# Kernel tuning notes

Measured on AMD Instinct MI355X. Metric: run time of the kernel, lower is better.

Reference implementation:

```python
import jax, jax.numpy as jnp
import numpy as np

ROTARY_BASE = 10000
INFTY_APPROX = 1e30
B, T, M, H, D = 2, 2048, 2048, 16, 128


def rope(x):
    # x: [B, T, H, D]; half-split rotary encoding
    *_, length, _, width = x.shape
    half = width // 2
    positions = jnp.arange(length, dtype=jnp.float32)[None, :, None, None]      # [1,T,1,1]
    dims = jnp.arange(half, dtype=jnp.float32)
    ang_freqs = jnp.power(float(ROTARY_BASE), -dims / half)[None, None, None, :]  # [1,1,1,D/2]
    radians = positions * ang_freqs
    cos = jnp.cos(radians).astype(x.dtype)
    sin = jnp.sin(radians).astype(x.dtype)
    even, odd = x[..., :half], x[..., half:]
    r_even = even * cos - odd * sin
    r_odd = even * sin + odd * cos
    return jnp.concatenate([r_even, r_odd], axis=-1)


def setup_inputs() -> dict:
    key = jax.random.key(0)
    k0, k1, k2, k3, k4 = jax.random.split(key, 5)
    return {
        "x": jax.random.normal(k0, (B, T, M), dtype=jnp.float32),
        "w_aq": jax.random.normal(k1, (H, M, D), dtype=jnp.float32) * (M ** -0.5),
        "w_ak": jax.random.normal(k2, (H, M, D), dtype=jnp.float32) * (M ** -0.5),
        "w_av": jax.random.normal(k3, (H, M, D), dtype=jnp.float32) * (M ** -0.5),
        "w_ao": jax.random.normal(k4, (H, D, M), dtype=jnp.float32) * ((2 * 24 * M) ** -0.5),
    }


def reference(x, w_aq, w_ak, w_av, w_ao):
    q = jnp.einsum("btm,hmd->bthd", x, w_aq)
    k = jnp.einsum("btm,hmd->bthd", x, w_ak)
    v = jnp.einsum("btm,hmd->bthd", x, w_av)
    q = rope(q)
    k = rope(k)
    # muP attention scaling: 1/d_head (not 1/sqrt(d_head))
    mult = (1.0 / D) ** 0.5
    s = jnp.einsum("bihd,bjhd->bhij", mult * q, mult * k)  # [B,H,T,T]
    i = jnp.arange(T)[:, None]
    j = jnp.arange(T)[None, :]
    mask = (i < j)[None, None, :, :]  # mask future positions
    s = s - jnp.asarray(INFTY_APPROX, dtype=x.dtype) * mask
    p = jax.nn.softmax(s, axis=-1)
    o = jnp.einsum("bhij,bjhd->bihd", p, v)
    r = jnp.einsum("bihd,hdm->bim", o, w_ao)
    return r
```

## Files before the change

kernel.cpp:

```cpp
#include <hip/hip_runtime.h>

#define Bb 2
#define Tt 2048
#define Mm 2048
#define Hh 16
#define Dd 128

typedef __attribute__((ext_vector_type(8))) short bf16x8;
typedef __attribute__((ext_vector_type(4))) float f32x4;
typedef __attribute__((ext_vector_type(16))) float f32x16;

__device__ __forceinline__ unsigned short f2bf(float f) {
    unsigned int u = __builtin_bit_cast(unsigned int, f);
    u += 0x7FFFu + ((u >> 16) & 1u);
    return (unsigned short)(u >> 16);
}

__device__ __forceinline__ unsigned int cvt_pk_bf16(float lo, float hi) {
    unsigned int r;
    asm("v_cvt_pk_bf16_f32 %0, %1, %2" : "=v"(r) : "v"(lo), "v"(hi));
    return r;
}

__device__ __forceinline__ float fexp2(float x) { return __builtin_amdgcn_exp2f(x); }

__device__ __forceinline__ void gld16(const void* g, void* l) {
    __builtin_amdgcn_global_load_lds(
        (const __attribute__((address_space(1))) void*)g,
        (__attribute__((address_space(3))) void*)l, 16, 0, 0);
}


__global__ __launch_bounds__(256) void cvt_x2(const float* __restrict__ x,
                                              unsigned short* __restrict__ xb2) {
    const int blk = blockIdx.x;
    const int mt = blk >> 5, kt = blk & 31;
#pragma unroll
    for (int it = 0; it < 4; ++it) {
        int s = it * 256 + threadIdx.x;
        int row = ((s >> 6) & 3) * 32 + (s & 31);
        int k = (s >> 8) * 16 + ((s >> 5) & 1) * 8;
        const float* sp = x + ((long)(mt * 128 + row)) * 2048 + kt * 64 + k;
        float4 a = *(const float4*)sp;
        float4 b = *(const float4*)(sp + 4);
        uint4 pk;
        pk.x = (unsigned int)f2bf(a.x) | ((unsigned int)f2bf(a.y) << 16);
        pk.y = (unsigned int)f2bf(a.z) | ((unsigned int)f2bf(a.w) << 16);
        pk.z = (unsigned int)f2bf(b.x) | ((unsigned int)f2bf(b.y) << 16);
        pk.w = (unsigned int)f2bf(b.z) | ((unsigned int)f2bf(b.w) << 16);
        *(uint4*)(xb2 + (((long)(mt * 32 + kt)) * 1024 + s) * 8) = pk;
    }
}

__global__ __launch_bounds__(256) void w_qkv_tile(
    const float* __restrict__ wq, const float* __restrict__ wk, const float* __restrict__ wv,
    unsigned short* __restrict__ outBase) {
    __shared__ float tile[64][132];
    const int kt = blockIdx.x;
    const int zy = blockIdx.y;
    const int which = zy >> 4, head = zy & 15;
    const float* src = (which == 0 ? wq : which == 1 ? wk : wv) + (long)head * 2048 * 128;
    const int tid = threadIdx.x;
#pragma unroll
    for (int it = 0; it < 8; ++it) {
        int f = it * 256 + tid;
        int row = f >> 5, c4 = f & 31;
        float4 v = *(const float4*)(src + (long)(kt * 64 + row) * 128 + c4 * 4);
        tile[row][c4 * 4 + 0] = v.x;
        tile[row][c4 * 4 + 1] = v.y;
        tile[row][c4 * 4 + 2] = v.z;
        tile[row][c4 * 4 + 3] = v.w;
    }
    __syncthreads();
    unsigned short* outp = outBase + (((long)(which * 16 + head)) * 32 + kt) * 1024 * 8;
#pragma unroll
    for (int it = 0; it < 4; ++it) {
        int up = it * 256 + tid;
        int kk = up >> 8, nf = (up >> 6) & 3, l = up & 63;
        int il = l & 31, hl = l >> 5;
        int d = il + 64 * (nf & 1) + 32 * (nf >> 1);
        int kl = kk * 16 + hl * 8;
        uint4 pk;
        pk.x = (unsigned int)f2bf(tile[kl + 0][d]) | ((unsigned int)f2bf(tile[kl + 1][d]) << 16);
        pk.y = (unsigned int)f2bf(tile[kl + 2][d]) | ((unsigned int)f2bf(tile[kl + 3][d]) << 16);
        pk.z = (unsigned int)f2bf(tile[kl + 4][d]) | ((unsigned int)f2bf(tile[kl + 5][d]) << 16);
        pk.w = (unsigned int)f2bf(tile[kl + 6][d]) | ((unsigned int)f2bf(tile[kl + 7][d]) << 16);
        *(uint4*)(outp + (long)up * 8) = pk;
    }
}

__global__ __launch_bounds__(256) void transpose_cvt(const float* __restrict__ in,
                                                     unsigned short* __restrict__ out,
                                                     int rows, int cols,
                                                     long in_slab, long out_slab) {
    __shared__ float tile[32][33];
    const float* ip = in + (long)blockIdx.z * in_slab;
    unsigned short* op = out + (long)blockIdx.z * out_slab;
    int r0 = blockIdx.x * 32, c0 = blockIdx.y * 32;
    int tx = threadIdx.x & 31, ty = threadIdx.x >> 5;
#pragma unroll
    for (int j = 0; j < 32; j += 8)
        tile[ty + j][tx] = ip[(long)(r0 + ty + j) * cols + c0 + tx];
    __syncthreads();
#pragma unroll
    for (int j = 0; j < 32; j += 8)
        op[(long)(c0 + ty + j) * rows + r0 + tx] = f2bf(tile[tx][ty + j]);
}

__global__ __launch_bounds__(256) void rope_tab(float* __restrict__ cosT,
                                                float* __restrict__ sinT) {
    int idx = blockIdx.x * 256 + threadIdx.x;
    int t = idx >> 6, d = idx & 63;
    float freq = powf(10000.f, -(float)d / 64.f);
    float ang = (float)t * freq;
    sinT[idx] = sinf(ang);
    cosT[idx] = cosf(ang);
}

template <bool WIDE>
__device__ __forceinline__ void proj_sub9(
    const unsigned short* __restrict__ xb2,
    const unsigned short* __restrict__ wT2,
    char* lds, int bm, int offc,
    unsigned short* __restrict__ qO, unsigned short* __restrict__ kO,
    unsigned short* __restrict__ vtO,
    const float* __restrict__ cosT, const float* __restrict__ sinT, int tid) {
    const int lane = tid & 63, wave = tid >> 6;
    const int il = lane & 31, hl = lane >> 5;
    const int wm = WIDE ? (wave >> 2) : (wave >> 1);
    const int wn = WIDE ? (wave & 3) : (wave & 1);
    const int hseg0 = offc >> 7;
    const int mode = offc >> 11;
    constexpr int MF = WIDE ? 4 : 2;
    constexpr int NFR = WIDE ? 12 : 8;
    constexpr int FS = WIDE ? 6 : 4;

    f32x16 acc[MF][2];
#pragma unroll
    for (int a = 0; a < MF; ++a)
#pragma unroll
        for (int b2 = 0; b2 < 2; ++b2)
#pragma unroll
            for (int e = 0; e < 16; ++e) acc[a][b2][e] = 0.f;

    auto stageTo = [&](int bufOff, int kt2) {
        const int kt = kt2 >> 1, hf = kt2 & 1;
        char* dst = lds + bufOff;
#pragma unroll
        for (int i = 0; i < 2; ++i) {
            int f = i * 512 + tid;
            int kk = f >> 9, rf = (f >> 6) & 7, l = f & 63;
            int mt = 2 * bm + (rf >> 2), rb = rf & 3;
            gld16(xb2 + (((long)(mt * 32 + kt)) * 1024 + (2 * hf + kk) * 256 + rb * 64 + l) * 8,
                  dst + f * 16);
        }
        if (WIDE) {
#pragma unroll
            for (int i = 0; i < 2; ++i) {
                int g = i * 512 + tid;
                int kk = g >> 9, cf = (g >> 6) & 7, l = g & 63;
                int hs = hseg0 + (cf >> 2), nf = cf & 3;
                gld16(wT2 + (((long)(hs * 32 + kt)) * 1024 + (2 * hf + kk) * 256 + nf * 64 + l) * 8,
                      dst + 16384 + g * 16);
            }
        } else {
            int g = tid;
            int kk = g >> 8, nf = (g >> 6) & 3, l = g & 63;
            gld16(wT2 + (((long)(hseg0 * 32 + kt)) * 1024 + (2 * hf + kk) * 256 + nf * 64 + l) * 8,
                  dst + 16384 + g * 16);
        }
    };

    auto prefetch = [&](bf16x8 (&fr)[NFR], int bufOff) {
        const char* bc = lds + bufOff;
#pragma unroll
        for (int kk2 = 0; kk2 < 2; ++kk2) {
#pragma unroll
            for (int mf = 0; mf < MF; ++mf)
                fr[kk2 * FS + mf] = *(const bf16x8*)(bc + (kk2 * 512 + (wm * MF + mf) * 64 + lane) * 16);
#pragma unroll
            for (int nf = 0; nf < 2; ++nf)
                fr[kk2 * FS + MF + nf] = *(const bf16x8*)(bc + 16384 +
                    ((WIDE ? kk2 * 512 : kk2 * 256) + (wn * 2 + nf) * 64 + lane) * 16);
        }
    };

    auto domfma = [&](bf16x8 (&fr)[NFR]) {
        __builtin_amdgcn_s_setprio(1);
#pragma unroll
        for (int kk2 = 0; kk2 < 2; ++kk2)
#pragma unroll
            for (int mf = 0; mf < MF; ++mf)
#pragma unroll
                for (int nf = 0; nf < 2; ++nf)
                    acc[mf][nf] = __builtin_amdgcn_mfma_f32_32x32x16_bf16(
                        fr[kk2 * FS + mf], fr[kk2 * FS + MF + nf], acc[mf][nf], 0, 0, 0);
        __builtin_amdgcn_s_setprio(0);
    };

    bf16x8 fA[NFR], fB[NFR];

    stageTo(0, 0);
    stageTo(32768, 1);
    if (WIDE) asm volatile("s_waitcnt vmcnt(4)" ::: "memory");
    else      asm volatile("s_waitcnt vmcnt(3)" ::: "memory");
    __builtin_amdgcn_s_barrier();
    prefetch(fA, 0);

    int curOff = 0;
    for (int p = 0; p < 31; ++p) {
        {
            int preOff = curOff + 65536; if (preOff >= 98304) preOff -= 98304;
            stageTo(preOff, 2 * p + 2);
            if (WIDE) asm volatile("s_waitcnt vmcnt(4) lgkmcnt(0)" ::: "memory");
            else      asm volatile("s_waitcnt vmcnt(3) lgkmcnt(0)" ::: "memory");
            __builtin_amdgcn_s_barrier();
            int nxtOff = curOff + 32768; if (nxtOff >= 98304) nxtOff -= 98304;
            prefetch(fB, nxtOff);
            domfma(fA);
            curOff = nxtOff;
        }
        {
            int preOff = curOff + 65536; if (preOff >= 98304) preOff -= 98304;
            stageTo(preOff, 2 * p + 3);
            if (WIDE) asm volatile("s_waitcnt vmcnt(4) lgkmcnt(0)" ::: "memory");
            else      asm volatile("s_waitcnt vmcnt(3) lgkmcnt(0)" ::: "memory");
            __builtin_amdgcn_s_barrier();
            int nxtOff = curOff + 32768; if (nxtOff >= 98304) nxtOff -= 98304;
            prefetch(fA, nxtOff);
            domfma(fB);
            curOff = nxtOff;
        }
    }
    asm volatile("s_waitcnt vmcnt(0) lgkmcnt(0)" ::: "memory");
    __builtin_amdgcn_s_barrier();
    {
        int nxtOff = curOff + 32768; if (nxtOff >= 98304) nxtOff -= 98304;
        prefetch(fB, nxtOff);
        domfma(fA);
    }
    domfma(fB);

    const int b = bm >> 3;
    const int t0 = (bm & 7) * 256;
    const int head_g = WIDE ? (hseg0 + (wn >> 1)) : hseg0;
    const int head_l = head_g & 15;
    const int opar = WIDE ? (wn & 1) : wn;
    constexpr int WMS = WIDE ? 128 : 64;

    if (mode < 2) {
        const float qs = (mode == 0) ? 0.011271055f : 1.0f;
        unsigned short* outp = (mode == 0) ? qO : kO;
        long hb = ((long)(b * Hh + head_l)) * Tt;
        int d_lo = il + 32 * opar;
#pragma unroll
        for (int mf = 0; mf < MF; ++mf)
#pragma unroll
            for (int reg = 0; reg < 16; ++reg) {
                int r = (reg & 3) + 8 * (reg >> 2) + 4 * hl;
                int tt = t0 + wm * WMS + mf * 32 + r;
                float c = cosT[tt * 64 + d_lo], s = sinT[tt * 64 + d_lo];
                float ev = acc[mf][0][reg], od = acc[mf][1][reg];
                long base = (hb + tt) * Dd;
                outp[base + d_lo]      = f2bf((ev * c - od * s) * qs);
                outp[base + d_lo + 64] = f2bf((ev * s + od * c) * qs);
            }
    } else {
        __syncthreads();
        char* patch = lds + wave * 4096;
        long hdbase = ((long)(b * Hh + head_l)) * Dd * Tt;
#pragma unroll
        for (int mf = 0; mf < MF; ++mf) {
#pragma unroll
            for (int nf = 0; nf < 2; ++nf) {
                int dslot = nf * 32 + il;
                int swz = (dslot & 3) << 4;
#pragma unroll
                for (int qg = 0; qg < 4; ++qg) {
                    uint2 w;
                    w.x = cvt_pk_bf16(acc[mf][nf][qg * 4 + 0], acc[mf][nf][qg * 4 + 1]);
                    w.y = cvt_pk_bf16(acc[mf][nf][qg * 4 + 2], acc[mf][nf][qg * 4 + 3]);
                    *(uint2*)(patch + dslot * 64 + ((qg * 16 + hl * 8) ^ swz)) = w;
                }
            }
            __builtin_amdgcn_s_waitcnt(0);
#pragma unroll
            for (int p2 = 0; p2 < 4; ++p2) {
                int dslot = p2 * 16 + (lane >> 2);
                int t8 = lane & 3;
                uint4 v = *(const uint4*)(patch + dslot * 64 + ((t8 * 16) ^ ((dslot & 3) << 4)));
                int o = opar * 2 + (dslot >> 5), il2 = dslot & 31;
                int dd = il2 + 32 * (o >> 1) + 64 * (o & 1);
                int tg = t0 + wm * WMS + mf * 32 + t8 * 8;
                *(uint4*)(vtO + hdbase + (long)dd * Tt + tg) = v;
            }
            __builtin_amdgcn_s_waitcnt(0);
        }
    }
}

__global__ __launch_bounds__(512, 2) void proj_gemm9(
    const unsigned short* __restrict__ xb2,
    const unsigned short* __restrict__ wT2,
    unsigned short* __restrict__ qO,
    unsigned short* __restrict__ kO,
    unsigned short* __restrict__ vtO,
    const float* __restrict__ cosT,
    const float* __restrict__ sinT) {
    __shared__ __align__(16) char lds[98304];
    const int bm = blockIdx.x;
    const int bc = blockIdx.y;
    const int s = bc * 384;
    const bool swap = ((s & 2047) == 1920);
    const int offw = swap ? s + 128 : s;
    const int offn = swap ? s : s + 256;
    const int tid = threadIdx.x;

    proj_sub9<true>(xb2, wT2, lds, bm, offw, qO, kO, vtO, cosT, sinT, tid);
    __syncthreads();
    proj_sub9<false>(xb2, wT2, lds, bm, offn, qO, kO, vtO, cosT, sinT, tid);
}

__global__ __launch_bounds__(256) void attn_kernel(
    const unsigned short* __restrict__ q,
    const unsigned short* __restrict__ k,
    const unsigned short* __restrict__ vt,
    unsigned short* __restrict__ o) {
    __shared__ __align__(16) unsigned short lds[32768];

    const int lid = (int)blockIdx.x;
    const int p = lid & 255;
    const int bh = p & 31;
    const int q0 = p >> 5;
    const int qb = (lid >> 8) ? (15 - q0) : q0;

    const int tid = threadIdx.x, lane = tid & 63, wave = tid >> 6;
    const int h = lane >> 5, iln = lane & 31;

    const unsigned short* qp = q + (long)bh * Tt * Dd;
    const unsigned short* kp = k + (long)bh * Tt * Dd;
    const unsigned short* vp = vt + (long)bh * Dd * Tt;

    const int i_g = qb * 128 + wave * 32 + iln;
    bf16x8 qf[8];
#pragma unroll
    for (int kk = 0; kk < 8; ++kk)
        qf[kk] = *(const bf16x8*)(qp + (long)i_g * Dd + kk * 16 + h * 8);

    f32x16 accO[4];
#pragma unroll
    for (int nb = 0; nb < 4; ++nb)
#pragma unroll
        for (int e = 0; e < 16; ++e) accO[nb][e] = 0.f;

    float m_r = -1e30f, l_r = 0.f;
    const int ntiles = 2 * qb + 2;

    auto stage = [&](int buf, int tix) {
        const int j0s = tix * 64;
#pragma unroll
        for (int it = 0; it < 4; ++it) {
            int f = it * 256 + tid;
            int rk = f >> 4, ck = f & 15;
            gld16(kp + ((long)(j0s + rk) * Dd + ((ck ^ (rk & 7)) << 3)),
                  (char*)lds + buf * 16384 + f * 16);
            int rv = f >> 3, cv = f & 7;
            gld16(vp + ((long)rv * Tt + j0s + ((cv ^ (rv & 7)) << 3)),
                  (char*)lds + 32768 + buf * 16384 + f * 16);
        }
    };

    stage(0, 0);

    for (int tix = 0; tix < ntiles; ++tix) {
        const int cur = tix & 1;
        const int j0 = tix * 64;
        if (tix + 1 < ntiles) {
            stage(cur ^ 1, tix + 1);
            asm volatile("s_waitcnt vmcnt(8)" ::: "memory");
        } else {
            asm volatile("s_waitcnt vmcnt(0)" ::: "memory");
        }
        __builtin_amdgcn_s_barrier();

        const char* Kb = (const char*)lds + cur * 16384;
        const char* Vb = (const char*)lds + 32768 + cur * 16384;

        f32x16 sacc[2];
#pragma unroll
        for (int mb = 0; mb < 2; ++mb)
#pragma unroll
            for (int e = 0; e < 16; ++e) sacc[mb][e] = 0.f;

        __builtin_amdgcn_s_setprio(1);
#pragma unroll
        for (int mb = 0; mb < 2; ++mb) {
            int row = mb * 32 + iln;
            const char* Kr = Kb + row * 256;
            int sw = row & 7;
#pragma unroll
            for (int kk = 0; kk < 8; ++kk) {
                bf16x8 kf = *(const bf16x8*)(Kr + 16 * ((kk * 2 + h) ^ sw));
                sacc[mb] = __builtin_amdgcn_mfma_f32_32x32x16_bf16(kf, qf[kk], sacc[mb], 0, 0, 0);
            }
        }
        __builtin_amdgcn_s_setprio(0);

        const bool domask = (j0 + 63 > qb * 128);
        if (domask) {
#pragma unroll
            for (int mb = 0; mb < 2; ++mb)
#pragma unroll
                for (int reg = 0; reg < 16; ++reg) {
                    int j = j0 + mb * 32 + (reg & 3) + 8 * (reg >> 2) + 4 * h;
                    if (j > i_g) sacc[mb][reg] = -1e30f;
                }
        }

        float red[16];
#pragma unroll
        for (int r = 0; r < 16; ++r) red[r] = fmaxf(sacc[0][r], sacc[1][r]);
#pragma unroll
        for (int s = 8; s >= 1; s >>= 1)
#pragma unroll
            for (int r = 0; r < s; ++r) red[r] = fmaxf(red[r], red[r + s]);
        float mx = fmaxf(red[0], __shfl_xor(red[0], 32, 64));

        if (__any(mx > m_r + 8.f)) {
            float mn = fmaxf(m_r, mx);
            float corr = fexp2(m_r - mn);
            m_r = mn;
            l_r *= corr;
#pragma unroll
            for (int reg = 0; reg < 16; ++reg) {
                int rrow = (reg & 3) + 8 * (reg >> 2) + 4 * h;
                float c = __shfl(corr, rrow, 64);
#pragma unroll
                for (int nb = 0; nb < 4; ++nb) accO[nb][reg] *= c;
            }
        }

        float pe[2][16];
#pragma unroll
        for (int mb = 0; mb < 2; ++mb)
#pragma unroll
            for (int r = 0; r < 16; ++r) pe[mb][r] = fexp2(sacc[mb][r] - m_r);
        float sr[16];
#pragma unroll
        for (int r = 0; r < 16; ++r) sr[r] = pe[0][r] + pe[1][r];
#pragma unroll
        for (int s = 8; s >= 1; s >>= 1)
#pragma unroll
            for (int r = 0; r < s; ++r) sr[r] += sr[r + s];
        l_r += sr[0] + __shfl_xor(sr[0], 32, 64);

        unsigned int pu[2][8];
#pragma unroll
        for (int mb = 0; mb < 2; ++mb)
#pragma unroll
            for (int t = 0; t < 8; ++t)
                pu[mb][t] = cvt_pk_bf16(pe[mb][2 * t], pe[mb][2 * t + 1]);

        unsigned int rv2[2][4];
#pragma unroll
        for (int mb = 0; mb < 2; ++mb)
#pragma unroll
            for (int u = 0; u < 4; ++u) {
                unsigned int sv = h ? pu[mb][(u & 1) + 4 * (u >> 1)]
                                    : pu[mb][2 + (u & 1) + 4 * (u >> 1)];
                rv2[mb][u] = __shfl_xor(sv, 32, 64);
            }

        __builtin_amdgcn_s_setprio(1);
#pragma unroll
        for (int kk2 = 0; kk2 < 4; ++kk2) {
            const int mb = kk2 >> 1, c2 = kk2 & 1;
            unsigned int w0 = h ? rv2[mb][2 * c2 + 0] : pu[mb][4 * c2 + 0];
            unsigned int w1 = h ? rv2[mb][2 * c2 + 1] : pu[mb][4 * c2 + 1];
            unsigned int w2 = h ? pu[mb][4 * c2 + 2] : rv2[mb][2 * c2 + 0];
            unsigned int w3 = h ? pu[mb][4 * c2 + 3] : rv2[mb][2 * c2 + 1];
            uint4 aw; aw.x = w0; aw.y = w1; aw.z = w2; aw.w = w3;
            bf16x8 af = __builtin_bit_cast(bf16x8, aw);
#pragma unroll
            for (int nb = 0; nb < 4; ++nb) {
                int dd = nb * 32 + iln;
                int byte = dd * 128 + 16 * ((kk2 * 2 + h) ^ (dd & 7));
                bf16x8 vf = *(const bf16x8*)(Vb + byte);
                accO[nb] = __builtin_amdgcn_mfma_f32_32x32x16_bf16(af, vf, accO[nb], 0, 0, 0);
            }
        }
        __builtin_amdgcn_s_setprio(0);

        asm volatile("" ::: "memory");
        __builtin_amdgcn_s_barrier();
    }

    const int b = bh >> 4, hh = bh & 15;
    float invl = 1.f / l_r;
#pragma unroll
    for (int reg = 0; reg < 16; ++reg) {
        int rrow = (reg & 3) + 8 * (reg >> 2) + 4 * h;
        float iv = __shfl(invl, rrow, 64);
        int t = qb * 128 + wave * 32 + rrow;
        long base = ((long)(b * Tt + t) * Hh + hh) * Dd;
#pragma unroll
        for (int nb = 0; nb < 4; ++nb)
            o[base + nb * 32 + iln] = f2bf(accO[nb][reg] * iv);
    }
}

__global__ __launch_bounds__(256) void out_gemm(
    const unsigned short* __restrict__ oIn,
    const unsigned short* __restrict__ woT,
    float* __restrict__ out) {
    __shared__ __align__(16) unsigned short smem[32768];
    const int bm = blockIdx.x, bn = blockIdx.y;
    const int tid = threadIdx.x;
    const int lane = tid & 63;
    const int wave = tid >> 6;
    const int g = lane >> 4;
    const int ln = lane & 15;

    const unsigned short* arow = oIn + (long)bm * 128 * Mm;
    const unsigned short* brow = woT + (long)bn * 128 * Mm;

    f32x4 acc[2][8];
#pragma unroll
    for (int a = 0; a < 2; ++a)
#pragma unroll
        for (int b2 = 0; b2 < 8; ++b2)
#pragma unroll
            for (int e = 0; e < 4; ++e) acc[a][b2][e] = 0.f;

    auto stage = [&](int buf, int kt) {
        const int k0 = kt * 64;
#pragma unroll
        for (int it = 0; it < 4; ++it) {
            int f = it * 256 + tid;
            int r = f >> 3, c = f & 7;
            long off = (long)r * Mm + k0 + ((c ^ (r & 7)) << 3);
            gld16(arow + off, (char*)smem + buf * 32768 + f * 16);
            gld16(brow + off, (char*)smem + buf * 32768 + 16384 + f * 16);
        }
    };

    stage(0, 0);

    for (int kt = 0; kt < Mm / 64; ++kt) {
        const int cur = kt & 1;
        asm volatile("s_waitcnt vmcnt(0)" ::: "memory");
        __builtin_amdgcn_s_barrier();
        if (kt + 1 < Mm / 64) stage(cur ^ 1, kt + 1);

        const char* Ab = (const char*)smem + cur * 32768;
        const char* Bv = Ab + 16384;
#pragma unroll
        for (int kc = 0; kc < 2; ++kc) {
            bf16x8 af[2];
#pragma unroll
            for (int rf = 0; rf < 2; ++rf) {
                int row = wave * 32 + rf * 16 + ln;
                int byte = (row * 128 + kc * 64 + g * 16) ^ ((row & 7) << 4);
                af[rf] = *(const bf16x8*)(Ab + byte);
            }
#pragma unroll
            for (int ni = 0; ni < 8; ++ni) {
                int row = ni * 16 + ln;
                int byte = (row * 128 + kc * 64 + g * 16) ^ ((row & 7) << 4);
                bf16x8 bfv = *(const bf16x8*)(Bv + byte);
#pragma unroll
                for (int rf = 0; rf < 2; ++rf)
                    acc[rf][ni] = __builtin_amdgcn_mfma_f32_16x16x32_bf16(af[rf], bfv, acc[rf][ni], 0, 0, 0);
            }
        }
        asm volatile("" ::: "memory");
    }

#pragma unroll
    for (int rf = 0; rf < 2; ++rf)
#pragma unroll
        for (int reg = 0; reg < 4; ++reg) {
            long row = bm * 128 + wave * 32 + rf * 16 + g * 4 + reg;
#pragma unroll
            for (int ni = 0; ni < 8; ++ni)
                out[row * Mm + bn * 128 + ni * 16 + ln] = acc[rf][ni][reg];
        }
}


extern "C" void kernel_launch(void* const* d_in, const int* in_sizes, int n_in,
                              void* d_out, int out_size, void* d_ws, size_t ws_size,
                              hipStream_t stream) {
    const float* x    = (const float*)d_in[0];
    const float* w_aq = (const float*)d_in[1];
    const float* w_ak = (const float*)d_in[2];
    const float* w_av = (const float*)d_in[3];
    const float* w_ao = (const float*)d_in[4];
    float* out = (float*)d_out;

    char* ws = (char*)d_ws;
    const long SZ_BTM = 16777216;
    const long SZ_W   = 8388608;
    unsigned short* xb2 = (unsigned short*)(ws);
    unsigned short* qB  = (unsigned short*)(ws + SZ_BTM);
    unsigned short* kB  = (unsigned short*)(ws + 2 * SZ_BTM);
    unsigned short* vtB = (unsigned short*)(ws + 3 * SZ_BTM);
    unsigned short* oB  = (unsigned short*)(ws + 4 * SZ_BTM);
    unsigned short* wT2 = (unsigned short*)(ws + 5 * SZ_BTM);
    unsigned short* woT = (unsigned short*)(ws + 5 * SZ_BTM + 3 * SZ_W);
    float* cosT = (float*)(ws + 5 * SZ_BTM + 4 * SZ_W);
    float* sinT = (float*)(ws + 5 * SZ_BTM + 4 * SZ_W + 524288);

    cvt_x2<<<1024, 256, 0, stream>>>(x, xb2);
    w_qkv_tile<<<dim3(32, 48), 256, 0, stream>>>(w_aq, w_ak, w_av, wT2);
    transpose_cvt<<<dim3(64, 64, 1), 256, 0, stream>>>(w_ao, woT, 2048, 2048, 0, 0);
    rope_tab<<<512, 256, 0, stream>>>(cosT, sinT);

    proj_gemm9<<<dim3(16, 16), 512, 0, stream>>>(xb2, wT2, qB, kB, vtB, cosT, sinT);
    attn_kernel<<<dim3(512), 256, 0, stream>>>(qB, kB, vtB, oB);
    out_gemm<<<dim3(32, 16), 256, 0, stream>>>(oB, woT, out);
}
```

Baseline: 251.4 us.

## Restructure projection GEMM to double-buffered full-K-tile staging with direct LDS fragment loads

Replaces the triple-buffered half-tile pipeline, which used register prefetch of MFMA fragments, with a two-stage double buffer that loads a full K-tile (64 k) per iteration into 128KB of LDS. Fragments are read from LDS right before each MFMA group instead of being ping-ponged in registers. The goal is to halve the number of barriers per K iteration and cut register pressure. In exchange it uses more LDS per block, which may limit occupancy to one block per CU despite launch_bounds(512,2). It also exposes LDS read latency, since fragment loads are no longer overlapped with the previous MFMAs.

```diff
diff --git a/kernel.cpp b/kernel.cpp
--- a/kernel.cpp
+++ b/kernel.cpp
@@ -118,7 +118,7 @@
 }
 
 template <bool WIDE>
-__device__ __forceinline__ void proj_sub9(
+__device__ __forceinline__ void proj_sub10(
     const unsigned short* __restrict__ xb2,
     const unsigned short* __restrict__ wT2,
     char* lds, int bm, int offc,
@@ -132,8 +132,6 @@
     const int hseg0 = offc >> 7;
     const int mode = offc >> 11;
     constexpr int MF = WIDE ? 4 : 2;
-    constexpr int NFR = WIDE ? 12 : 8;
-    constexpr int FS = WIDE ? 6 : 4;
 
     f32x16 acc[MF][2];
 #pragma unroll
@@ -143,103 +141,73 @@
 #pragma unroll
             for (int e = 0; e < 16; ++e) acc[a][b2][e] = 0.f;
 
-    auto stageTo = [&](int bufOff, int kt2) {
-        const int kt = kt2 >> 1, hf = kt2 & 1;
-        char* dst = lds + bufOff;
-#pragma unroll
-        for (int i = 0; i < 2; ++i) {
+    auto stageTo = [&](int buf, int kt) {
+        char* dst = lds + buf * 65536;
+#pragma unroll
+        for (int i = 0; i < 4; ++i) {
             int f = i * 512 + tid;
-            int kk = f >> 9, rf = (f >> 6) & 7, l = f & 63;
-            int mt = 2 * bm + (rf >> 2), rb = rf & 3;
-            gld16(xb2 + (((long)(mt * 32 + kt)) * 1024 + (2 * hf + kk) * 256 + rb * 64 + l) * 8,
-                  dst + f * 16);
+            int sub = f >> 10, s = f & 1023;
+            gld16(xb2 + (((long)((2 * bm + sub) * 32 + kt)) * 1024 + s) * 8, dst + f * 16);
         }
         if (WIDE) {
+#pragma unroll
+            for (int i = 0; i < 4; ++i) {
+                int g = i * 512 + tid;
+                int hs = g >> 10, u = g & 1023;
+                gld16(wT2 + (((long)((hseg0 + hs) * 32 + kt)) * 1024 + u) * 8,
+                      dst + 32768 + g * 16);
+            }
+        } else {
 #pragma unroll
             for (int i = 0; i < 2; ++i) {
                 int g = i * 512 + tid;
-                int kk = g >> 9, cf = (g >> 6) & 7, l = g & 63;
-                int hs = hseg0 + (cf >> 2), nf = cf & 3;
-                gld16(wT2 + (((long)(hs * 32 + kt)) * 1024 + (2 * hf + kk) * 256 + nf * 64 + l) * 8,
-                      dst + 16384 + g * 16);
-            }
+                gld16(wT2 + (((long)(hseg0 * 32 + kt)) * 1024 + g) * 8,
+                      dst + 32768 + g * 16);
+            }
+        }
+    };
+
+    stageTo(0, 0);
+
+    for (int t = 0; t < 32; ++t) {
+        const int cur = t & 1;
+        if (t + 1 < 32) {
+            stageTo(cur ^ 1, t + 1);
+            if (WIDE) asm volatile("s_waitcnt vmcnt(8)" ::: "memory");
+            else      asm volatile("s_waitcnt vmcnt(6)" ::: "memory");
         } else {
-            int g = tid;
-            int kk = g >> 8, nf = (g >> 6) & 3, l = g & 63;
-            gld16(wT2 + (((long)(hseg0 * 32 + kt)) * 1024 + (2 * hf + kk) * 256 + nf * 64 + l) * 8,
-                  dst + 16384 + g * 16);
-        }
-    };
-
-    auto prefetch = [&](bf16x8 (&fr)[NFR], int bufOff) {
-        const char* bc = lds + bufOff;
-#pragma unroll
-        for (int kk2 = 0; kk2 < 2; ++kk2) {
+            asm volatile("s_waitcnt vmcnt(0)" ::: "memory");
+        }
+        __builtin_amdgcn_s_barrier();
+
+        const char* bc = lds + cur * 65536;
+        __builtin_amdgcn_s_setprio(1);
+#pragma unroll
+        for (int kk = 0; kk < 4; ++kk) {
+            bf16x8 af[MF], bf[2];
+#pragma unroll
+            for (int mf = 0; mf < MF; ++mf) {
+                int chunk = WIDE ? (wm * 1024 + kk * 256 + mf * 64 + lane)
+                                 : ((wm >> 1) * 1024 + kk * 256 + ((wm & 1) * 2 + mf) * 64 + lane);
+                af[mf] = *(const bf16x8*)(bc + chunk * 16);
+            }
+#pragma unroll
+            for (int nf2 = 0; nf2 < 2; ++nf2) {
+                int chunk = WIDE ? ((wn >> 1) * 1024 + kk * 256 + ((wn & 1) * 2 + nf2) * 64 + lane)
+                                 : (kk * 256 + (wn * 2 + nf2) * 64 + lane);
+                bf[nf2] = *(const bf16x8*)(bc + 32768 + chunk * 16);
+            }
 #pragma unroll
             for (int mf = 0; mf < MF; ++mf)
-                fr[kk2 * FS + mf] = *(const bf16x8*)(bc + (kk2 * 512 + (wm * MF + mf) * 64 + lane) * 16);
-#pragma unroll
-            for (int nf = 0; nf < 2; ++nf)
-                fr[kk2 * FS + MF + nf] = *(const bf16x8*)(bc + 16384 +
-                    ((WIDE ? kk2 * 512 : kk2 * 256) + (wn * 2 + nf) * 64 + lane) * 16);
-        }
-    };
-
-    auto domfma = [&](bf16x8 (&fr)[NFR]) {
-        __builtin_amdgcn_s_setprio(1);
-#pragma unroll
-        for (int kk2 = 0; kk2 < 2; ++kk2)
-#pragma unroll
-            for (int mf = 0; mf < MF; ++mf)
-#pragma unroll
-                for (int nf = 0; nf < 2; ++nf)
-                    acc[mf][nf] = __builtin_amdgcn_mfma_f32_32x32x16_bf16(
-                        fr[kk2 * FS + mf], fr[kk2 * FS + MF + nf], acc[mf][nf], 0, 0, 0);
+#pragma unroll
+                for (int nf2 = 0; nf2 < 2; ++nf2)
+                    acc[mf][nf2] = __builtin_amdgcn_mfma_f32_32x32x16_bf16(
+                        af[mf], bf[nf2], acc[mf][nf2], 0, 0, 0);
+        }
         __builtin_amdgcn_s_setprio(0);
-    };
-
-    bf16x8 fA[NFR], fB[NFR];
-
-    stageTo(0, 0);
-    stageTo(32768, 1);
-    if (WIDE) asm volatile("s_waitcnt vmcnt(4)" ::: "memory");
-    else      asm volatile("s_waitcnt vmcnt(3)" ::: "memory");
-    __builtin_amdgcn_s_barrier();
-    prefetch(fA, 0);
-
-    int curOff = 0;
-    for (int p = 0; p < 31; ++p) {
-        {
-            int preOff = curOff + 65536; if (preOff >= 98304) preOff -= 98304;
-            stageTo(preOff, 2 * p + 2);
-            if (WIDE) asm volatile("s_waitcnt vmcnt(4) lgkmcnt(0)" ::: "memory");
-            else      asm volatile("s_waitcnt vmcnt(3) lgkmcnt(0)" ::: "memory");
-            __builtin_amdgcn_s_barrier();
-            int nxtOff = curOff + 32768; if (nxtOff >= 98304) nxtOff -= 98304;
-            prefetch(fB, nxtOff);
-            domfma(fA);
-            curOff = nxtOff;
-        }
-        {
-            int preOff = curOff + 65536; if (preOff >= 98304) preOff -= 98304;
-            stageTo(preOff, 2 * p + 3);
-            if (WIDE) asm volatile("s_waitcnt vmcnt(4) lgkmcnt(0)" ::: "memory");
-            else      asm volatile("s_waitcnt vmcnt(3) lgkmcnt(0)" ::: "memory");
-            __builtin_amdgcn_s_barrier();
-            int nxtOff = curOff + 32768; if (nxtOff >= 98304) nxtOff -= 98304;
-            prefetch(fA, nxtOff);
-            domfma(fB);
-            curOff = nxtOff;
-        }
-    }
-    asm volatile("s_waitcnt vmcnt(0) lgkmcnt(0)" ::: "memory");
-    __builtin_amdgcn_s_barrier();
-    {
-        int nxtOff = curOff + 32768; if (nxtOff >= 98304) nxtOff -= 98304;
-        prefetch(fB, nxtOff);
-        domfma(fA);
-    }
-    domfma(fB);
+        asm volatile("" ::: "memory");
+        __builtin_amdgcn_s_barrier();
+    }
 
     const int b = bm >> 3;
     const int t0 = (bm & 7) * 256;
@@ -299,7 +267,7 @@
     }
 }
 
-__global__ __launch_bounds__(512, 2) void proj_gemm9(
+__global__ __launch_bounds__(512, 2) void proj_gemm10(
     const unsigned short* __restrict__ xb2,
     const unsigned short* __restrict__ wT2,
     unsigned short* __restrict__ qO,
@@ -307,7 +275,7 @@
     unsigned short* __restrict__ vtO,
     const float* __restrict__ cosT,
     const float* __restrict__ sinT) {
-    __shared__ __align__(16) char lds[98304];
+    __shared__ __align__(16) char lds[131072];
     const int bm = blockIdx.x;
     const int bc = blockIdx.y;
     const int s = bc * 384;
@@ -316,9 +284,9 @@
     const int offn = swap ? s : s + 256;
     const int tid = threadIdx.x;
 
-    proj_sub9<true>(xb2, wT2, lds, bm, offw, qO, kO, vtO, cosT, sinT, tid);
+    proj_sub10<true>(xb2, wT2, lds, bm, offw, qO, kO, vtO, cosT, sinT, tid);
     __syncthreads();
-    proj_sub9<false>(xb2, wT2, lds, bm, offn, qO, kO, vtO, cosT, sinT, tid);
+    proj_sub10<false>(xb2, wT2, lds, bm, offn, qO, kO, vtO, cosT, sinT, tid);
 }
 
 __global__ __launch_bounds__(256) void attn_kernel(
@@ -616,7 +584,7 @@
     transpose_cvt<<<dim3(64, 64, 1), 256, 0, stream>>>(w_ao, woT, 2048, 2048, 0, 0);
     rope_tab<<<512, 256, 0, stream>>>(cosT, sinT);
 
-    proj_gemm9<<<dim3(16, 16), 512, 0, stream>>>(xb2, wT2, qB, kB, vtB, cosT, sinT);
+    proj_gemm10<<<dim3(16, 16), 512, 0, stream>>>(xb2, wT2, qB, kB, vtB, cosT, sinT);
     attn_kernel<<<dim3(512), 256, 0, stream>>>(qB, kB, vtB, oB);
     out_gemm<<<dim3(32, 16), 256, 0, stream>>>(oB, woT, out);
 }
```

Result: faster. 242.1 us (-3.7%).
